# Kernel tuning notes

Measured on AMD Instinct MI355X. Metric: run time of the kernel, lower is better.

The kernel has to match this reference:

```python
import jax, jax.numpy as jnp
import numpy as np

B, N, D, H = 4, 2048, 1024, 16
DH = D // H


def setup_inputs() -> dict:
    key = jax.random.key(0)
    k_x, k_q, k_k, k_v, k_o = jax.random.split(key, 5)
    s = 1.0 / np.sqrt(D)
    return {
        "x": jax.random.normal(k_x, (B, N, D), dtype=jnp.float32),
        "mask": jnp.ones((B, N), dtype=bool),
        "Wq": jax.random.normal(k_q, (D, D), dtype=jnp.float32) * s,
        "Wk": jax.random.normal(k_k, (D, D), dtype=jnp.float32) * s,
        "Wv": jax.random.normal(k_v, (D, D), dtype=jnp.float32) * s,
        "Wo": jax.random.normal(k_o, (D, D), dtype=jnp.float32) * s,
    }


def reference(x, mask, Wq, Wk, Wv, Wo):
    # nn.Linear(bias=False): y = x @ W.T ; weights stored [out, in]
    q = jnp.einsum("bnd,ed->bne", x, Wq)
    k = jnp.einsum("bnd,ed->bne", x, Wk)
    v = jnp.einsum("bnd,ed->bne", x, Wv)
    # split heads: [b, n, d] -> [b, h, n, dh]
    def split(t):
        return t.reshape(B, N, H, DH).transpose(0, 2, 1, 3)
    q, k, v = split(q), split(k), split(v)
    # naive scaled dot-product attention (mask is dead code in the source)
    scores = jnp.einsum("bhnd,bhmd->bhnm", q, k) / jnp.sqrt(jnp.float32(DH))
    attn = jax.nn.softmax(scores, axis=-1)
    out = jnp.einsum("bhnm,bhmd->bhnd", attn, v)  # [b, h, n, dh]
    # merge heads: [b, h, n, dh] -> [b, n, d]
    out = out.transpose(0, 2, 1, 3).reshape(B, N, D)
    return jnp.einsum("bnd,ed->bne", out, Wo)
```

## Files before the change

kernel.cpp:

```cpp
#include <hip/hip_runtime.h>
#include <math.h>

constexpr int Bc  = 4;
constexpr int Nc  = 2048;
constexpr int Dc  = 1024;
constexpr int Hc  = 16;
constexpr int DHc = 64;
constexpr int Mrows = Bc * Nc;

typedef unsigned short ushortT;
typedef __attribute__((ext_vector_type(8))) short bf16x8;
typedef __attribute__((ext_vector_type(4))) unsigned short u16x4;
typedef __attribute__((ext_vector_type(4))) float f32x4;

#define QSCALE 0.18033688011112043f

#define GLD_LDS16(g, l)                                                        \
  __builtin_amdgcn_global_load_lds(                                            \
      (const __attribute__((address_space(1))) void*)(g),                      \
      (__attribute__((address_space(3))) void*)(l), 16, 0, 0)

__device__ inline ushortT f2bf(float f) {
  unsigned int u = __float_as_uint(f);
  u += 0x7fffu + ((u >> 16) & 1u);
  return (ushortT)(u >> 16);
}

__device__ inline float fexp2(float x) { return __builtin_amdgcn_exp2f(x); }

__global__ __launch_bounds__(256) void cvt_kernel(
    const float* __restrict__ x, const float* __restrict__ wq,
    const float* __restrict__ wk, const float* __restrict__ wv,
    const float* __restrict__ wo, ushortT* __restrict__ dst) {
  const int g = blockIdx.x * 256 + threadIdx.x;
  const float* src;
  size_t soff, doff;
  if (g < 2097152) {
    src = x;
    soff = (size_t)g * 4;
    doff = soff;
  } else {
    const int t = g - 2097152;
    const int w = t >> 18;
    const int off = t & 262143;
    src = (w == 0) ? wq : (w == 1) ? wk : (w == 2) ? wv : wo;
    soff = (size_t)off * 4;
    doff = 8388608u + (size_t)w * 1048576u + (size_t)off * 4;
  }
  float4 v = *(const float4*)(src + soff);
  ushort4 o = make_ushort4(f2bf(v.x), f2bf(v.y), f2bf(v.z), f2bf(v.w));
  *(ushort4*)(dst + doff) = o;
}

template <int QKV>
__global__ __launch_bounds__(256) void mfma_gemm(const ushortT* __restrict__ A,
                                                 const ushortT* __restrict__ W0,
                                                 void* __restrict__ C0) {
  __shared__ ushortT As[2][128 * 32];
  __shared__ ushortT Bs[2][128 * 32];

  const int tid = threadIdx.x;
  const int wave = tid >> 6, lane = tid & 63;
  const int quad = lane >> 4, lrow = lane & 15;
  const int bx = blockIdx.x, by = blockIdx.y;
  const int wsel = QKV ? (bx >> 3) : 0;
  const int e0 = QKV ? ((bx & 7) * 128) : (bx * 128);
  const int m0 = by * 128;
  const ushortT* Wp = W0 + (size_t)wsel * (Dc * Dc);
  const float oscale = (QKV && wsel == 0) ? QSCALE : 1.0f;

  const ushortT* ag = A  + (size_t)(m0 + wave * 32 + (lane >> 2)) * Dc + (lane & 3) * 8;
  const ushortT* bg = Wp + (size_t)(e0 + wave * 32 + (lane >> 2)) * Dc + (lane & 3) * 8;
  const int lbase = wave * 1024 + lane * 8;

  f32x4 acc[4][4];
#pragma unroll
  for (int i = 0; i < 4; ++i)
#pragma unroll
    for (int j = 0; j < 4; ++j) acc[i][j] = (f32x4){0.f, 0.f, 0.f, 0.f};

  const int wm = (wave >> 1) * 64, wn = (wave & 1) * 64;

  for (int k0 = 0; k0 < Dc; k0 += 64) {
    __syncthreads();
#pragma unroll
    for (int p = 0; p < 2; ++p) {
      GLD_LDS16(ag + p * 32, &As[p][lbase]);
      GLD_LDS16(ag + p * 32 + 16 * Dc, &As[p][lbase + 512]);
      GLD_LDS16(bg + p * 32, &Bs[p][lbase]);
      GLD_LDS16(bg + p * 32 + 16 * Dc, &Bs[p][lbase + 512]);
    }
    ag += 64;
    bg += 64;
    __syncthreads();

#pragma unroll
    for (int p = 0; p < 2; ++p) {
      bf16x8 af[4], bf[4];
#pragma unroll
      for (int mt = 0; mt < 4; ++mt)
        af[mt] = *(const bf16x8*)(&As[p][(wm + mt * 16 + lrow) * 32 + quad * 8]);
#pragma unroll
      for (int nt = 0; nt < 4; ++nt)
        bf[nt] = *(const bf16x8*)(&Bs[p][(wn + nt * 16 + lrow) * 32 + quad * 8]);
#pragma unroll
      for (int mt = 0; mt < 4; ++mt)
#pragma unroll
        for (int nt = 0; nt < 4; ++nt)
          acc[mt][nt] = __builtin_amdgcn_mfma_f32_16x16x32_bf16(
              af[mt], bf[nt], acc[mt][nt], 0, 0, 0);
    }
  }

#pragma unroll
  for (int mt = 0; mt < 4; ++mt) {
#pragma unroll
    for (int nt = 0; nt < 4; ++nt) {
#pragma unroll
      for (int r = 0; r < 4; ++r) {
        const int m = m0 + wm + mt * 16 + quad * 4 + r;
        const int e = e0 + wn + nt * 16 + lrow;
        const float v = acc[mt][nt][r] * oscale;
        if (QKV) {
          const int b = m >> 11, n = m & 2047;
          const int h = e >> 6, dh = e & 63;
          ushortT* C = (ushortT*)C0 + (size_t)wsel * ((size_t)Mrows * Dc);
          C[(((size_t)(b * Hc + h)) * Nc + n) * DHc + dh] = f2bf(v);
        } else {
          ((float*)C0)[(size_t)m * Dc + e] = v;
        }
      }
    }
  }
}

__global__ __launch_bounds__(256, 2) void attn_mfma(const ushortT* __restrict__ Q,
                                                    const ushortT* __restrict__ K,
                                                    const ushortT* __restrict__ V,
                                                    ushortT* __restrict__ O) {
  __shared__ ushortT smemA[256 * 72];
  __shared__ ushortT Ks[2][64 * 64];
  __shared__ ushortT Vt[64 * 72];

  const int tid = threadIdx.x;
  const int wave = tid >> 6, lane = tid & 63;
  const int quad = lane >> 4, lrow = lane & 15;
  const int bh = blockIdx.y;
  const int q0 = blockIdx.x * 256;

  const ushortT* qg = Q + (size_t)bh * Nc * DHc;
  const ushortT* kg = K + (size_t)bh * Nc * DHc;
  const ushortT* vg = V + (size_t)bh * Nc * DHc;

  const int kq = tid & 15;
  const int dhg = (tid >> 4) * 4;

#pragma unroll
  for (int c = 0; c < 2; ++c)
#pragma unroll
    for (int rh = 0; rh < 4; ++rh) {
      const int row = wave * 64 + rh * 16;
      GLD_LDS16(qg + (size_t)(q0 + row + (lane >> 2)) * DHc + c * 32 + (lane & 3) * 8,
                smemA + (c * 256 + row) * 32 + lane * 8);
    }
#pragma unroll
  for (int i = 0; i < 2; ++i) {
    const int cid = wave * 2 + i;
    const int c = cid & 1, kb = (cid >> 1) * 16;
    GLD_LDS16(kg + (size_t)(kb + (lane >> 2)) * DHc + c * 32 + (lane & 3) * 8,
              &Ks[0][(c * 64 + kb) * 32 + lane * 8]);
  }
  u16x4 vreg[4];
#pragma unroll
  for (int g = 0; g < 4; ++g)
    vreg[g] = *(const u16x4*)(vg + (size_t)(kq + 16 * g) * DHc + dhg);

  __syncthreads();

  bf16x8 af_q[4][2];
#pragma unroll
  for (int mt = 0; mt < 4; ++mt)
#pragma unroll
    for (int ks = 0; ks < 2; ++ks)
      af_q[mt][ks] = *(const bf16x8*)(smemA +
          ((ks * 256 + wave * 64 + mt * 16 + lrow) * 32 + quad * 8));

  {
    ushortT tmp[4][4];
#pragma unroll
    for (int g = 0; g < 4; ++g)
#pragma unroll
      for (int d = 0; d < 4; ++d) tmp[d][g] = vreg[g][d];
#pragma unroll
    for (int d = 0; d < 4; ++d)
      *(u16x4*)(Vt + (dhg + d) * 72 + kq * 4) = *(const u16x4*)tmp[d];
  }
  __syncthreads();

  f32x4 o_acc[4][4];
#pragma unroll
  for (int mt = 0; mt < 4; ++mt)
#pragma unroll
    for (int nt = 0; nt < 4; ++nt) o_acc[mt][nt] = (f32x4){0.f, 0.f, 0.f, 0.f};
  float l_i[16];
#pragma unroll
  for (int i = 0; i < 16; ++i) l_i[i] = 0.f;

  for (int k0 = 0; k0 < Nc; k0 += 64) {
    const int cur = (k0 >> 6) & 1, nxt = cur ^ 1;
    const bool pref = (k0 + 64 < Nc);

    if (pref) {
#pragma unroll
      for (int i = 0; i < 2; ++i) {
        const int cid = wave * 2 + i;
        const int c = cid & 1, kb = (cid >> 1) * 16;
        GLD_LDS16(kg + (size_t)(k0 + 64 + kb + (lane >> 2)) * DHc + c * 32 + (lane & 3) * 8,
                  &Ks[nxt][(c * 64 + kb) * 32 + lane * 8]);
      }
#pragma unroll
      for (int g = 0; g < 4; ++g)
        vreg[g] = *(const u16x4*)(vg + (size_t)(k0 + 64 + kq + 16 * g) * DHc + dhg);
    }

    bf16x8 bf_k[4][2];
#pragma unroll
    for (int nt = 0; nt < 4; ++nt)
#pragma unroll
      for (int ks = 0; ks < 2; ++ks)
        bf_k[nt][ks] = *(const bf16x8*)(&Ks[cur][(ks * 64 + nt * 16 + lrow) * 32 + quad * 8]);

    f32x4 s_acc[4][4];
#pragma unroll
    for (int mt = 0; mt < 4; ++mt)
#pragma unroll
      for (int nt = 0; nt < 4; ++nt) {
        s_acc[mt][nt] = (f32x4){0.f, 0.f, 0.f, 0.f};
#pragma unroll
        for (int ks = 0; ks < 2; ++ks)
          s_acc[mt][nt] = __builtin_amdgcn_mfma_f32_16x16x32_bf16(
              af_q[mt][ks], bf_k[nt][ks], s_acc[mt][nt], 0, 0, 0);
      }

#pragma unroll
    for (int mt = 0; mt < 4; ++mt) {
#pragma unroll
      for (int r = 0; r < 4; ++r) {
        const float p0 = fexp2(s_acc[mt][0][r]);
        const float p1 = fexp2(s_acc[mt][1][r]);
        const float p2 = fexp2(s_acc[mt][2][r]);
        const float p3 = fexp2(s_acc[mt][3][r]);
        l_i[mt * 4 + r] += (p0 + p1) + (p2 + p3);
        const unsigned pk01 = __builtin_amdgcn_perm(
            __float_as_uint(p1), __float_as_uint(p0), 0x07060302u);
        const unsigned pk23 = __builtin_amdgcn_perm(
            __float_as_uint(p3), __float_as_uint(p2), 0x07060302u);
        const int row = wave * 64 + mt * 16 + quad * 4 + r;
        *(uint2*)(smemA + row * 72 + lrow * 4) = make_uint2(pk01, pk23);
      }
    }
    asm volatile("s_waitcnt lgkmcnt(0)" ::: "memory");

    bf16x8 af_p[4][2], bf_v[4][2];
#pragma unroll
    for (int mt = 0; mt < 4; ++mt)
#pragma unroll
      for (int ks = 0; ks < 2; ++ks)
        af_p[mt][ks] = *(const bf16x8*)(smemA +
            (wave * 64 + mt * 16 + lrow) * 72 + ks * 32 + quad * 8);
#pragma unroll
    for (int nt = 0; nt < 4; ++nt)
#pragma unroll
      for (int ks = 0; ks < 2; ++ks)
        bf_v[nt][ks] = *(const bf16x8*)(Vt + (nt * 16 + lrow) * 72 + ks * 32 + quad * 8);
#pragma unroll
    for (int mt = 0; mt < 4; ++mt)
#pragma unroll
      for (int nt = 0; nt < 4; ++nt)
#pragma unroll
        for (int ks = 0; ks < 2; ++ks)
          o_acc[mt][nt] = __builtin_amdgcn_mfma_f32_16x16x32_bf16(
              af_p[mt][ks], bf_v[nt][ks], o_acc[mt][nt], 0, 0, 0);

    __syncthreads();

    if (pref) {
      ushortT tmp[4][4];
#pragma unroll
      for (int g = 0; g < 4; ++g)
#pragma unroll
        for (int d = 0; d < 4; ++d) tmp[d][g] = vreg[g][d];
#pragma unroll
      for (int d = 0; d < 4; ++d)
        *(u16x4*)(Vt + (dhg + d) * 72 + kq * 4) = *(const u16x4*)tmp[d];
    }

    __syncthreads();
  }

#pragma unroll
  for (int i = 0; i < 16; ++i) {
    float s = l_i[i];
#pragma unroll
    for (int off = 8; off >= 1; off >>= 1) s += __shfl_xor(s, off, 16);
    l_i[i] = s;
  }

  const int b = bh / Hc, h = bh % Hc;
#pragma unroll
  for (int mt = 0; mt < 4; ++mt) {
#pragma unroll
    for (int r = 0; r < 4; ++r) {
      const float inv_l = 1.0f / l_i[mt * 4 + r];
      const int n = q0 + wave * 64 + mt * 16 + quad * 4 + r;
      const size_t base = ((size_t)b * Nc + n) * Dc + h * DHc;
#pragma unroll
      for (int nt = 0; nt < 4; ++nt)
        O[base + nt * 16 + lrow] = f2bf(o_acc[mt][nt][r] * inv_l);
    }
  }
}

extern "C" void kernel_launch(void* const* d_in, const int* in_sizes, int n_in,
                              void* d_out, int out_size, void* d_ws,
                              size_t ws_size, hipStream_t stream) {
  const float* x  = (const float*)d_in[0];
  const float* Wq = (const float*)d_in[2];
  const float* Wk = (const float*)d_in[3];
  const float* Wv = (const float*)d_in[4];
  const float* Wo = (const float*)d_in[5];

  ushortT* ws16 = (ushortT*)d_ws;
  ushortT* xb   = ws16;
  ushortT* wqb  = xb + (size_t)Mrows * Dc;
  ushortT* qkvb = wqb + 4 * (size_t)Dc * Dc;
  ushortT* qb   = qkvb;
  ushortT* kb   = qb + (size_t)Mrows * Dc;
  ushortT* vb   = kb + (size_t)Mrows * Dc;
  ushortT* aob  = vb + (size_t)Mrows * Dc;
  ushortT* wob  = wqb + 3 * (size_t)Dc * Dc;

  dim3 blk(256);
  hipLaunchKernelGGL(cvt_kernel, dim3(12288), blk, 0, stream, x, Wq, Wk, Wv, Wo,
                     ws16);

  hipLaunchKernelGGL((mfma_gemm<1>), dim3(24, Mrows / 128), blk, 0, stream, xb,
                     wqb, (void*)qkvb);

  hipLaunchKernelGGL(attn_mfma, dim3(Nc / 256, Bc * Hc), blk, 0, stream, qb,
                     kb, vb, aob);

  hipLaunchKernelGGL((mfma_gemm<0>), dim3(8, Mrows / 128), blk, 0, stream, aob,
                     wob, d_out);
}
```

Measured before the change: 276.5 us.

## Split attention block across 8 waves, double-buffer V tile, swizzle K LDS

```diff
diff --git a/kernel.cpp b/kernel.cpp
--- a/kernel.cpp
+++ b/kernel.cpp
@@ -10,6 +10,7 @@
 
 typedef unsigned short ushortT;
 typedef __attribute__((ext_vector_type(8))) short bf16x8;
+typedef __attribute__((ext_vector_type(2))) unsigned short u16x2;
 typedef __attribute__((ext_vector_type(4))) unsigned short u16x4;
 typedef __attribute__((ext_vector_type(4))) float f32x4;
 
@@ -134,13 +135,13 @@
   }
 }
 
-__global__ __launch_bounds__(256, 2) void attn_mfma(const ushortT* __restrict__ Q,
+__global__ __launch_bounds__(512, 4) void attn_mfma(const ushortT* __restrict__ Q,
                                                     const ushortT* __restrict__ K,
                                                     const ushortT* __restrict__ V,
                                                     ushortT* __restrict__ O) {
   __shared__ ushortT smemA[256 * 72];
   __shared__ ushortT Ks[2][64 * 64];
-  __shared__ ushortT Vt[64 * 72];
+  __shared__ ushortT Vt[2][64 * 72];
 
   const int tid = threadIdx.x;
   const int wave = tid >> 6, lane = tid & 63;
@@ -152,75 +153,69 @@
   const ushortT* kg = K + (size_t)bh * Nc * DHc;
   const ushortT* vg = V + (size_t)bh * Nc * DHc;
 
+  const int ksw = (lane & 3) ^ ((lane >> 3) & 3);
+  const int krd = (lrow >> 1) & 3;
+
+  const int kc = wave & 1, kb = (wave >> 1) * 16;
+  const int krow = kb + (lane >> 2);
+
   const int kq = tid & 15;
-  const int dhg = (tid >> 4) * 4;
+  const int dhg = ((tid >> 4) & 15) * 4;
+  const int kh = tid >> 8;
 
 #pragma unroll
   for (int c = 0; c < 2; ++c)
 #pragma unroll
-    for (int rh = 0; rh < 4; ++rh) {
-      const int row = wave * 64 + rh * 16;
+    for (int rh = 0; rh < 2; ++rh) {
+      const int row = wave * 32 + rh * 16;
       GLD_LDS16(qg + (size_t)(q0 + row + (lane >> 2)) * DHc + c * 32 + (lane & 3) * 8,
                 smemA + (c * 256 + row) * 32 + lane * 8);
     }
-#pragma unroll
-  for (int i = 0; i < 2; ++i) {
-    const int cid = wave * 2 + i;
-    const int c = cid & 1, kb = (cid >> 1) * 16;
-    GLD_LDS16(kg + (size_t)(kb + (lane >> 2)) * DHc + c * 32 + (lane & 3) * 8,
-              &Ks[0][(c * 64 + kb) * 32 + lane * 8]);
-  }
-  u16x4 vreg[4];
-#pragma unroll
-  for (int g = 0; g < 4; ++g)
-    vreg[g] = *(const u16x4*)(vg + (size_t)(kq + 16 * g) * DHc + dhg);
+  GLD_LDS16(kg + (size_t)krow * DHc + kc * 32 + ksw * 8,
+            &Ks[0][(kc * 64 + kb) * 32 + lane * 8]);
+  u16x4 vreg[2];
+#pragma unroll
+  for (int j = 0; j < 2; ++j)
+    vreg[j] = *(const u16x4*)(vg + (size_t)(kq + 16 * j + 32 * kh) * DHc + dhg);
 
   __syncthreads();
 
-  bf16x8 af_q[4][2];
-#pragma unroll
-  for (int mt = 0; mt < 4; ++mt)
+  bf16x8 af_q[2][2];
+#pragma unroll
+  for (int mt = 0; mt < 2; ++mt)
 #pragma unroll
     for (int ks = 0; ks < 2; ++ks)
       af_q[mt][ks] = *(const bf16x8*)(smemA +
-          ((ks * 256 + wave * 64 + mt * 16 + lrow) * 32 + quad * 8));
-
-  {
-    ushortT tmp[4][4];
-#pragma unroll
-    for (int g = 0; g < 4; ++g)
-#pragma unroll
-      for (int d = 0; d < 4; ++d) tmp[d][g] = vreg[g][d];
-#pragma unroll
-    for (int d = 0; d < 4; ++d)
-      *(u16x4*)(Vt + (dhg + d) * 72 + kq * 4) = *(const u16x4*)tmp[d];
+          ((ks * 256 + wave * 32 + mt * 16 + lrow) * 32 + quad * 8));
+
+#pragma unroll
+  for (int d = 0; d < 4; ++d) {
+    u16x2 t;
+    t[0] = vreg[0][d];
+    t[1] = vreg[1][d];
+    *(u16x2*)(&Vt[0][(dhg + d) * 72 + kq * 4 + kh * 2]) = t;
   }
   __syncthreads();
 
-  f32x4 o_acc[4][4];
-#pragma unroll
-  for (int mt = 0; mt < 4; ++mt)
+  f32x4 o_acc[2][4];
+#pragma unroll
+  for (int mt = 0; mt < 2; ++mt)
 #pragma unroll
     for (int nt = 0; nt < 4; ++nt) o_acc[mt][nt] = (f32x4){0.f, 0.f, 0.f, 0.f};
-  float l_i[16];
-#pragma unroll
-  for (int i = 0; i < 16; ++i) l_i[i] = 0.f;
+  float l_i[8];
+#pragma unroll
+  for (int i = 0; i < 8; ++i) l_i[i] = 0.f;
 
   for (int k0 = 0; k0 < Nc; k0 += 64) {
     const int cur = (k0 >> 6) & 1, nxt = cur ^ 1;
     const bool pref = (k0 + 64 < Nc);
 
     if (pref) {
-#pragma unroll
-      for (int i = 0; i < 2; ++i) {
-        const int cid = wave * 2 + i;
-        const int c = cid & 1, kb = (cid >> 1) * 16;
-        GLD_LDS16(kg + (size_t)(k0 + 64 + kb + (lane >> 2)) * DHc + c * 32 + (lane & 3) * 8,
-                  &Ks[nxt][(c * 64 + kb) * 32 + lane * 8]);
-      }
-#pragma unroll
-      for (int g = 0; g < 4; ++g)
-        vreg[g] = *(const u16x4*)(vg + (size_t)(k0 + 64 + kq + 16 * g) * DHc + dhg);
+      GLD_LDS16(kg + (size_t)(k0 + 64 + krow) * DHc + kc * 32 + ksw * 8,
+                &Ks[nxt][(kc * 64 + kb) * 32 + lane * 8]);
+#pragma unroll
+      for (int j = 0; j < 2; ++j)
+        vreg[j] = *(const u16x4*)(vg + (size_t)(k0 + 64 + kq + 16 * j + 32 * kh) * DHc + dhg);
     }
 
     bf16x8 bf_k[4][2];
@@ -228,11 +223,12 @@
     for (int nt = 0; nt < 4; ++nt)
 #pragma unroll
       for (int ks = 0; ks < 2; ++ks)
-        bf_k[nt][ks] = *(const bf16x8*)(&Ks[cur][(ks * 64 + nt * 16 + lrow) * 32 + quad * 8]);
-
-    f32x4 s_acc[4][4];
-#pragma unroll
-    for (int mt = 0; mt < 4; ++mt)
+        bf_k[nt][ks] = *(const bf16x8*)(
+            &Ks[cur][(ks * 64 + nt * 16 + lrow) * 32 + (quad ^ krd) * 8]);
+
+    f32x4 s_acc[2][4];
+#pragma unroll
+    for (int mt = 0; mt < 2; ++mt)
 #pragma unroll
       for (int nt = 0; nt < 4; ++nt) {
         s_acc[mt][nt] = (f32x4){0.f, 0.f, 0.f, 0.f};
@@ -243,7 +239,7 @@
       }
 
 #pragma unroll
-    for (int mt = 0; mt < 4; ++mt) {
+    for (int mt = 0; mt < 2; ++mt) {
 #pragma unroll
       for (int r = 0; r < 4; ++r) {
         const float p0 = fexp2(s_acc[mt][0][r]);
@@ -255,26 +251,27 @@
             __float_as_uint(p1), __float_as_uint(p0), 0x07060302u);
         const unsigned pk23 = __builtin_amdgcn_perm(
             __float_as_uint(p3), __float_as_uint(p2), 0x07060302u);
-        const int row = wave * 64 + mt * 16 + quad * 4 + r;
+        const int row = wave * 32 + mt * 16 + quad * 4 + r;
         *(uint2*)(smemA + row * 72 + lrow * 4) = make_uint2(pk01, pk23);
       }
     }
     asm volatile("s_waitcnt lgkmcnt(0)" ::: "memory");
 
-    bf16x8 af_p[4][2], bf_v[4][2];
-#pragma unroll
-    for (int mt = 0; mt < 4; ++mt)
+    bf16x8 af_p[2][2], bf_v[4][2];
+#pragma unroll
+    for (int mt = 0; mt < 2; ++mt)
 #pragma unroll
       for (int ks = 0; ks < 2; ++ks)
         af_p[mt][ks] = *(const bf16x8*)(smemA +
-            (wave * 64 + mt * 16 + lrow) * 72 + ks * 32 + quad * 8);
+            (wave * 32 + mt * 16 + lrow) * 72 + ks * 32 + quad * 8);
 #pragma unroll
     for (int nt = 0; nt < 4; ++nt)
 #pragma unroll
       for (int ks = 0; ks < 2; ++ks)
-        bf_v[nt][ks] = *(const bf16x8*)(Vt + (nt * 16 + lrow) * 72 + ks * 32 + quad * 8);
-#pragma unroll
-    for (int mt = 0; mt < 4; ++mt)
+        bf_v[nt][ks] = *(const bf16x8*)(
+            &Vt[cur][(nt * 16 + lrow) * 72 + ks * 32 + quad * 8]);
+#pragma unroll
+    for (int mt = 0; mt < 2; ++mt)
 #pragma unroll
       for (int nt = 0; nt < 4; ++nt)
 #pragma unroll
@@ -282,24 +279,21 @@
           o_acc[mt][nt] = __builtin_amdgcn_mfma_f32_16x16x32_bf16(
               af_p[mt][ks], bf_v[nt][ks], o_acc[mt][nt], 0, 0, 0);
 
+    if (pref) {
+#pragma unroll
+      for (int d = 0; d < 4; ++d) {
+        u16x2 t;
+        t[0] = vreg[0][d];
+        t[1] = vreg[1][d];
+        *(u16x2*)(&Vt[nxt][(dhg + d) * 72 + kq * 4 + kh * 2]) = t;
+      }
+    }
+
     __syncthreads();
-
-    if (pref) {
-      ushortT tmp[4][4];
-#pragma unroll
-      for (int g = 0; g < 4; ++g)
-#pragma unroll
-        for (int d = 0; d < 4; ++d) tmp[d][g] = vreg[g][d];
-#pragma unroll
-      for (int d = 0; d < 4; ++d)
-        *(u16x4*)(Vt + (dhg + d) * 72 + kq * 4) = *(const u16x4*)tmp[d];
-    }
-
-    __syncthreads();
-  }
-
-#pragma unroll
-  for (int i = 0; i < 16; ++i) {
+  }
+
+#pragma unroll
+  for (int i = 0; i < 8; ++i) {
     float s = l_i[i];
 #pragma unroll
     for (int off = 8; off >= 1; off >>= 1) s += __shfl_xor(s, off, 16);
@@ -308,11 +302,11 @@
 
   const int b = bh / Hc, h = bh % Hc;
 #pragma unroll
-  for (int mt = 0; mt < 4; ++mt) {
+  for (int mt = 0; mt < 2; ++mt) {
 #pragma unroll
     for (int r = 0; r < 4; ++r) {
       const float inv_l = 1.0f / l_i[mt * 4 + r];
-      const int n = q0 + wave * 64 + mt * 16 + quad * 4 + r;
+      const int n = q0 + wave * 32 + mt * 16 + quad * 4 + r;
       const size_t base = ((size_t)b * Nc + n) * Dc + h * DHc;
 #pragma unroll
       for (int nt = 0; nt < 4; ++nt)
@@ -347,8 +341,8 @@
   hipLaunchKernelGGL((mfma_gemm<1>), dim3(24, Mrows / 128), blk, 0, stream, xb,
                      wqb, (void*)qkvb);
 
-  hipLaunchKernelGGL(attn_mfma, dim3(Nc / 256, Bc * Hc), blk, 0, stream, qb,
-                     kb, vb, aob);
+  hipLaunchKernelGGL(attn_mfma, dim3(Nc / 256, Bc * Hc), dim3(512), 0, stream,
+                     qb, kb, vb, aob);
 
   hipLaunchKernelGGL((mfma_gemm<0>), dim3(8, Mrows / 128), blk, 0, stream, aob,
                      wob, d_out);
```

Result: slower. 335.2 us (+21.2%).
